# Kernel optimization log

Hardware: AMD Instinct MI355X
Metric: run time of the kernel (lower is better)

Reference implementation:

```python
import jax, jax.numpy as jnp
import numpy as np

B, T = 1, 2048
N_EMBD = 2048
N_HEAD = 16
HEAD_DIM = 128
Q_COMP = 1536
KV_COMP = 512
ROT = 64  # rotate_dim


def setup_inputs() -> dict:
    key = jax.random.key(0)
    ks = jax.random.split(key, 12)
    nrm = lambda k, shp, sc=1.0: jax.random.normal(k, shp, jnp.float32) * sc
    return {
        "x": nrm(ks[0], (B, T, N_EMBD)),
        "cos": jax.random.uniform(ks[1], (T, ROT // 2), jnp.float32),
        "sin": jax.random.uniform(ks[2], (T, ROT // 2), jnp.float32),
        "Wq_d_w": nrm(ks[3], (Q_COMP, N_EMBD), 0.02),
        "Wq_d_b": jnp.zeros((Q_COMP,), jnp.float32),
        "Wkv_d_w": nrm(ks[4], (KV_COMP, N_EMBD), 0.02),
        "Wq_u_w": nrm(ks[5], (N_HEAD * HEAD_DIM, Q_COMP), 0.02),
        "Wk_u_w": nrm(ks[6], (N_HEAD * HEAD_DIM, KV_COMP), 0.02),
        "Wv_u_w": nrm(ks[7], (N_HEAD * HEAD_DIM, KV_COMP), 0.02),
        "W_qr_w": nrm(ks[8], (N_HEAD * ROT, Q_COMP), 0.02),
        "W_kr_w": nrm(ks[9], (ROT, N_EMBD), 0.02),
        "W_out_w": nrm(ks[10], (N_EMBD, N_HEAD * HEAD_DIM), 0.02),
    }


def _rope(x, cos, sin):
    # x: [B, H, T, r]; cos/sin: [T, r//2] broadcast over batch and heads
    d = x.shape[-1] // 2
    x1, x2 = x[..., :d], x[..., d:]
    return jnp.concatenate([x1 * cos + x2 * sin, -x1 * sin + x2 * cos], axis=-1)


def reference(x, cos, sin, Wq_d_w, Wq_d_b, Wkv_d_w, Wq_u_w, Wk_u_w, Wv_u_w, W_qr_w, W_kr_w, W_out_w):
    Bn, Tn, _ = x.shape
    cq = x @ Wq_d_w.T + Wq_d_b           # [B,T,Qc] latent query
    ckv = x @ Wkv_d_w.T                  # [B,T,Kc] compressed KV latent (= K_t = V)
    Wq_u = Wq_u_w.reshape(N_HEAD, HEAD_DIM, Q_COMP)
    Wk_u = Wk_u_w.reshape(N_HEAD, HEAD_DIM, KV_COMP)
    Wv_u = Wv_u_w.reshape(N_HEAD, HEAD_DIM, KV_COMP)
    # absorbed per-head W_qk[h] = Wq_u_h^T @ Wk_u_h : [H, Qc, Kc]
    W_qk = jnp.einsum('hdq,hdk->hqk', Wq_u, Wk_u)
    Q_t = jnp.einsum('btq,hqk->bhtk', cq, W_qk)   # [B,H,T,Kc] content query in latent space
    Q_r = _rope(jnp.einsum('btq,hrq->bhtr', cq, W_qr_w.reshape(N_HEAD, ROT, Q_COMP)), cos, sin)
    K_r = _rope((x @ W_kr_w.T)[:, None], cos, sin)  # [B,1,T,R] single shared rotary key head
    Q = jnp.concatenate([Q_t, Q_r], axis=-1)        # [B,H,T,Kc+R]
    K = jnp.concatenate([ckv[:, None], K_r], axis=-1)  # [B,1,T,Kc+R]
    scale = 1.0 / np.sqrt(KV_COMP + ROT).astype(np.float32)
    scores = jnp.einsum('bhqd,bokd->bhqk', Q, K) * scale  # [B,H,T,T]
    causal = jnp.tril(jnp.ones((Tn, Tn), dtype=bool))
    scores = jnp.where(causal, scores, jnp.asarray(-1e30, scores.dtype))
    probs = jax.nn.softmax(scores, axis=-1)
    attn = jnp.einsum('bhqk,bkc->bhqc', probs, ckv)  # [B,H,T,Kc] latent attention output
    # absorbed output projection: up-project per head via Wv_u, then W_out
    heads = jnp.einsum('bhtc,hdc->bthd', attn, Wv_u).reshape(Bn, Tn, N_HEAD * HEAD_DIM)
    return heads @ W_out_w.T                          # [B,T,C]
```

## Files before the change

kernel.cpp:

```cpp
#include <hip/hip_runtime.h>
#include <math.h>
#include <stdint.h>
#include <stddef.h>

typedef __bf16 bf16;
typedef __bf16 bf16x8 __attribute__((ext_vector_type(8)));
typedef __bf16 bf16x4 __attribute__((ext_vector_type(4)));
typedef __bf16 bf16x2 __attribute__((ext_vector_type(2)));
typedef float  f32x4  __attribute__((ext_vector_type(4)));
typedef float  f32x4v __attribute__((ext_vector_type(4)));

typedef __attribute__((address_space(1))) const void* as1cv;
typedef __attribute__((address_space(3))) void*       as3v;

__device__ __forceinline__ f32x4 mfma16(bf16x8 a, bf16x8 b, f32x4 c) {
  return __builtin_amdgcn_mfma_f32_16x16x32_bf16(a, b, c, 0, 0, 0);
}

__device__ __forceinline__ void gload_lds16(const bf16* g, bf16* l) {
  __builtin_amdgcn_global_load_lds((as1cv)g, (as3v)l, 16, 0, 0);
}

struct CvtTable {
  const float* s[9];
  bf16* d[9];
  int cum[10];
};

__global__ void cvt_all(CvtTable T, int total4) {
  int i = blockIdx.x * blockDim.x + threadIdx.x;
  int stride = gridDim.x * blockDim.x;
  for (; i < total4; i += stride) {
    int k = 0;
#pragma unroll
    for (int j = 1; j < 9; ++j) k += (i >= T.cum[j]) ? 1 : 0;
    int off = i - T.cum[k];
    f32x4v v = ((const f32x4v*)T.s[k])[off];
    bf16x4 o;
    o[0] = (bf16)v[0]; o[1] = (bf16)v[1]; o[2] = (bf16)v[2]; o[3] = (bf16)v[3];
    ((bf16x4*)T.d[k])[off] = o;
  }
}

__device__ __forceinline__ void gemm_core(
    const bf16* __restrict__ A, int lda,
    const bf16* __restrict__ B, int K,
    float* __restrict__ Cf, bf16* __restrict__ Cb, int ldc,
    const float* __restrict__ bias, int bias_n, int m0, int n0)
{
  __shared__ __align__(16) bf16 Al[2][128 * 64];
  __shared__ __align__(16) bf16 Bl[2][128 * 64];
  const int tid = threadIdx.x;
  const int l = tid & 63;
  const int wid = tid >> 6;
  const int wr = wid >> 1, wc = wid & 1;
  const int lr = l & 15, lg = l >> 4;

  auto STAGE = [&](int b, int k0) {
#pragma unroll
    for (int it = 0; it < 4; ++it) {
      int chunk = it * 256 + tid;
      int row = chunk >> 3;
      int scb = (chunk & 7) ^ (row & 7);
      gload_lds16(A + (size_t)(m0 + row) * lda + k0 + scb * 8, &Al[b][chunk * 8]);
    }
#pragma unroll
    for (int it = 0; it < 4; ++it) {
      int chunk = it * 256 + tid;
      int row = chunk >> 3;
      int scb = (chunk & 7) ^ (row & 7);
      gload_lds16(B + (size_t)(n0 + row) * K + k0 + scb * 8, &Bl[b][chunk * 8]);
    }
  };

  f32x4 z = {0.f, 0.f, 0.f, 0.f};
  f32x4 acc[4][4];
#pragma unroll
  for (int i = 0; i < 4; ++i)
#pragma unroll
    for (int j = 0; j < 4; ++j) acc[i][j] = z;

  STAGE(0, 0);
  __syncthreads();
  int cur = 0;
  for (int k0 = 0; k0 < K; k0 += 64) {
    if (k0 + 64 < K) STAGE(cur ^ 1, k0 + 64);
#pragma unroll
    for (int kk = 0; kk < 2; ++kk) {
      bf16x8 af[4], bfr[4];
#pragma unroll
      for (int i = 0; i < 4; ++i) {
        int row = wr * 64 + i * 16 + lr;
        int cq = kk * 4 + lg;
        af[i] = *(const bf16x8*)(&Al[cur][row * 64 + ((cq ^ (row & 7)) * 8)]);
      }
#pragma unroll
      for (int j = 0; j < 4; ++j) {
        int row = wc * 64 + j * 16 + lr;
        int cq = kk * 4 + lg;
        bfr[j] = *(const bf16x8*)(&Bl[cur][row * 64 + ((cq ^ (row & 7)) * 8)]);
      }
#pragma unroll
      for (int i = 0; i < 4; ++i)
#pragma unroll
        for (int j = 0; j < 4; ++j)
          acc[i][j] = mfma16(af[i], bfr[j], acc[i][j]);
    }
    __syncthreads();
    cur ^= 1;
  }

#pragma unroll
  for (int i = 0; i < 4; ++i)
#pragma unroll
    for (int j = 0; j < 4; ++j)
#pragma unroll
      for (int r = 0; r < 4; ++r) {
        int row = m0 + wr * 64 + i * 16 + lg * 4 + r;
        int col = n0 + wc * 64 + j * 16 + lr;
        float v = acc[i][j][r];
        if (bias != nullptr && col < bias_n) v += bias[col];
        if (Cf != nullptr) Cf[(size_t)row * ldc + col] = v;
        else               Cb[(size_t)row * ldc + col] = (bf16)v;
      }
}

template<bool OUTF32>
__global__ __launch_bounds__(256) void gemm_bt(
    const bf16* __restrict__ A, int lda,
    const bf16* __restrict__ B, int K,
    float* __restrict__ Cf, bf16* __restrict__ Cb, int ldc,
    const float* __restrict__ bias, int bias_n)
{
  gemm_core(A, lda, B, K, OUTF32 ? Cf : nullptr, Cb, ldc, bias, bias_n,
            blockIdx.y * 128, blockIdx.x * 128);
}

__global__ __launch_bounds__(256) void gemm_bt_dual(
    const bf16* __restrict__ A0, int lda0, const bf16* __restrict__ B0, int K0,
    bf16* __restrict__ C0, int ldc0, int nbx0,
    const bf16* __restrict__ A1, int lda1, const bf16* __restrict__ B1, int K1,
    bf16* __restrict__ C1, int ldc1, int nbx1)
{
  int bid = blockIdx.x;
  if (bid < nbx0 * 16) {
    gemm_core(A0, lda0, B0, K0, nullptr, C0, ldc0, nullptr, 0,
              (bid / nbx0) * 128, (bid % nbx0) * 128);
  } else {
    bid -= nbx0 * 16;
    gemm_core(A1, lda1, B1, K1, nullptr, C1, ldc1, nullptr, 0,
              (bid / nbx1) * 128, (bid % nbx1) * 128);
  }
}

__global__ void rope_tv(const bf16* __restrict__ QA, const bf16* __restrict__ c_all,
                        const float* __restrict__ cosb, const float* __restrict__ sinb,
                        bf16* __restrict__ Qr, bf16* __restrict__ Kr,
                        const bf16* __restrict__ KV, bf16* __restrict__ Vt)
{
  int bid = blockIdx.x;
  if (bid < 2048) {
    int t = bid;
    for (int idx = threadIdx.x; idx < 544; idx += 256) {
      if (idx < 512) {
        int h = idx >> 5, p = idx & 31;
        float x1 = (float)QA[(size_t)t * 3072 + 2048 + h * 64 + p];
        float x2 = (float)QA[(size_t)t * 3072 + 2048 + h * 64 + 32 + p];
        float c = cosb[t * 32 + p], s = sinb[t * 32 + p];
        Qr[(size_t)t * 1024 + h * 64 + p]      = (bf16)( x1 * c + x2 * s);
        Qr[(size_t)t * 1024 + h * 64 + 32 + p] = (bf16)(-x1 * s + x2 * c);
      } else {
        int p = idx - 512;
        float x1 = (float)c_all[(size_t)t * 2176 + 2048 + p];
        float x2 = (float)c_all[(size_t)t * 2176 + 2048 + 32 + p];
        float c = cosb[t * 32 + p], s = sinb[t * 32 + p];
        Kr[(size_t)t * 64 + p]      = (bf16)( x1 * c + x2 * s);
        Kr[(size_t)t * 64 + 32 + p] = (bf16)(-x1 * s + x2 * c);
      }
    }
  } else {
    __shared__ bf16 tile[32][33];
    int tb = bid - 2048;
    int t0 = (tb & 63) * 32, c0 = (tb >> 6) * 32;
    int tx = threadIdx.x & 31, ty = threadIdx.x >> 5;
#pragma unroll
    for (int r = 0; r < 4; ++r)
      tile[ty + r * 8][tx] = KV[(size_t)(t0 + ty + r * 8) * 4096 + 2048 + c0 + tx];
    __syncthreads();
#pragma unroll
    for (int r = 0; r < 4; ++r)
      Vt[(size_t)(c0 + ty + r * 8) * 2048 + t0 + tx] = tile[tx][ty + r * 8];
  }
}

__global__ __launch_bounds__(256) void attn_kernel(
    const bf16* __restrict__ QA,
    const bf16* __restrict__ Qr,
    const bf16* __restrict__ KV,
    const bf16* __restrict__ Kr,
    const bf16* __restrict__ Vt,
    bf16* __restrict__ heads)
{
  __shared__ __align__(16) bf16 Kl[2][32 * 128];
  __shared__ __align__(16) bf16 Krl[2][32 * 64];
  __shared__ __align__(16) bf16 Vl[2][128 * 32];
  __shared__ __align__(16) bf16 Pl[4][16][40];

  const int tid = threadIdx.x;
  const int l = tid & 63;
  const int wid = tid >> 6;
  const int lr = l & 15, lg = l >> 4;

  const int wg = blockIdx.x;
  const int xcd = wg & 7, inx = wg >> 3;
  const int half = inx >> 5, j = inx & 31;
  const int h = xcd * 2 + half;
  const int qb = half ? j : 31 - j;
  const int q0 = qb * 64 + wid * 16;
  const int q = q0 + lr;

  const float scale = 0.041666666666666664f;
  f32x4 z = {0.f, 0.f, 0.f, 0.f};

  auto STAGE = [&](int b, int s0) {
#pragma unroll
    for (int it = 0; it < 2; ++it) {
      int ch = it * 256 + tid;
      int r = ch >> 4, p = ch & 15;
      int cb = (p & 8) | ((p & 7) ^ (r & 7));
      gload_lds16(&KV[(size_t)(s0 + r) * 4096 + h * 128 + cb * 8], &Kl[b][ch * 8]);
    }
    {
      int ch = tid;
      int r = ch >> 3, p = ch & 7;
      int cb = p ^ (r & 7);
      gload_lds16(&Kr[(size_t)(s0 + r) * 64 + cb * 8], &Krl[b][ch * 8]);
    }
#pragma unroll
    for (int it = 0; it < 2; ++it) {
      int ch = it * 256 + tid;
      int r = ch >> 2, p = ch & 3;
      int cb = p ^ ((r >> 1) & 3);
      gload_lds16(&Vt[(size_t)(h * 128 + r) * 2048 + s0 + cb * 8], &Vl[b][ch * 8]);
    }
  };

  bf16x8 aq[6];
#pragma unroll
  for (int kc = 0; kc < 4; ++kc)
    aq[kc] = *(const bf16x8*)&QA[(size_t)q * 3072 + h * 128 + kc * 32 + lg * 8];
#pragma unroll
  for (int kc = 4; kc < 6; ++kc)
    aq[kc] = *(const bf16x8*)&Qr[(size_t)q * 1024 + h * 64 + (kc - 4) * 32 + lg * 8];

  float m_run = -1e30f, l_run = 0.f;
  f32x4 acc[8];
#pragma unroll
  for (int c = 0; c < 8; ++c) acc[c] = z;

  const int nIter = 2 * qb + 2;
  STAGE(0, 0);
  __syncthreads();
  int cur = 0;
  for (int st = 0; st < nIter; ++st) {
    const int s0 = st * 32;
    if (st + 1 < nIter) STAGE(cur ^ 1, s0 + 32);
    if (s0 <= q0 + 15) {
      f32x4 sc[2];
      sc[0] = z; sc[1] = z;
#pragma unroll
      for (int t = 0; t < 2; ++t) {
        const int rr = t * 16 + lr;
#pragma unroll
        for (int kc = 0; kc < 4; ++kc) {
          int g = kc * 4 + lg;
          bf16x8 ka = *(const bf16x8*)&Kl[cur][rr * 128 + (((g & 8) | ((g & 7) ^ (rr & 7))) * 8)];
          sc[t] = mfma16(ka, aq[kc], sc[t]);
        }
#pragma unroll
        for (int kc = 4; kc < 6; ++kc) {
          int g = (kc - 4) * 4 + lg;
          bf16x8 ka = *(const bf16x8*)&Krl[cur][rr * 64 + ((g ^ (rr & 7)) * 8)];
          sc[t] = mfma16(ka, aq[kc], sc[t]);
        }
      }
      float pv[2][4];
      float mx = -1e30f;
#pragma unroll
      for (int t = 0; t < 2; ++t)
#pragma unroll
        for (int r = 0; r < 4; ++r) {
          int k = s0 + t * 16 + lg * 4 + r;
          float v = sc[t][r] * scale;
          if (k > q) v = -1e30f;
          pv[t][r] = v;
          mx = fmaxf(mx, v);
        }
      mx = fmaxf(mx, __shfl_xor(mx, 16, 64));
      mx = fmaxf(mx, __shfl_xor(mx, 32, 64));
      float mnew = fmaxf(m_run, mx);
      float alpha = __expf(m_run - mnew);
      float sum = 0.f;
#pragma unroll
      for (int t = 0; t < 2; ++t)
#pragma unroll
        for (int r = 0; r < 4; ++r) {
          float e = __expf(pv[t][r] - mnew);
          pv[t][r] = e;
          sum += e;
        }
      sum += __shfl_xor(sum, 16, 64);
      sum += __shfl_xor(sum, 32, 64);
      l_run = l_run * alpha + sum;
      m_run = mnew;
#pragma unroll
      for (int c = 0; c < 8; ++c)
#pragma unroll
        for (int r = 0; r < 4; ++r) acc[c][r] *= alpha;
#pragma unroll
      for (int t = 0; t < 2; ++t)
#pragma unroll
        for (int hf = 0; hf < 2; ++hf) {
          bf16x2 w;
          w[0] = (bf16)pv[t][2 * hf];
          w[1] = (bf16)pv[t][2 * hf + 1];
          *(bf16x2*)&Pl[wid][lr][t * 16 + lg * 4 + 2 * hf] = w;
        }
      bf16x8 pa = *(const bf16x8*)&Pl[wid][lr][lg * 8];
#pragma unroll
      for (int c = 0; c < 8; ++c) {
        int rv = c * 16 + lr;
        bf16x8 va = *(const bf16x8*)&Vl[cur][rv * 32 + ((lg ^ ((rv >> 1) & 3)) * 8)];
        acc[c] = mfma16(va, pa, acc[c]);
      }
    }
    __syncthreads();
    cur ^= 1;
  }

  const float inv = 1.f / l_run;
#pragma unroll
  for (int c = 0; c < 8; ++c) {
    bf16x4 o;
#pragma unroll
    for (int r = 0; r < 4; ++r) o[r] = (bf16)(acc[c][r] * inv);
    *(bf16x4*)&heads[(size_t)q * 2048 + h * 128 + c * 16 + lg * 4] = o;
  }
}

extern "C" void kernel_launch(void* const* d_in, const int* in_sizes, int n_in,
                              void* d_out, int out_size, void* d_ws, size_t ws_size,
                              hipStream_t stream) {
  (void)in_sizes; (void)n_in; (void)out_size; (void)ws_size;
  const float* x      = (const float*)d_in[0];
  const float* cosp   = (const float*)d_in[1];
  const float* sinp   = (const float*)d_in[2];
  const float* Wq_d   = (const float*)d_in[3];
  const float* Wq_d_b = (const float*)d_in[4];
  const float* Wkv_d  = (const float*)d_in[5];
  const float* Wq_u   = (const float*)d_in[6];
  const float* Wk_u   = (const float*)d_in[7];
  const float* Wv_u   = (const float*)d_in[8];
  const float* W_qr   = (const float*)d_in[9];
  const float* W_kr   = (const float*)d_in[10];
  const float* W_out  = (const float*)d_in[11];

  char* ws = (char*)d_ws;
  size_t off = 0;
  auto alloc = [&](size_t bytes) {
    char* p = ws + off;
    off += (bytes + 255) & ~(size_t)255;
    return p;
  };
  bf16* xb    = (bf16*)alloc((size_t)2048 * 2048 * 2);
  bf16* Wcat  = (bf16*)alloc((size_t)2176 * 2048 * 2);
  bf16* c_all = (bf16*)alloc((size_t)2048 * 2176 * 2);
  bf16* Wqu   = (bf16*)alloc((size_t)3072 * 1536 * 2);
  bf16* QA    = (bf16*)alloc((size_t)2048 * 3072 * 2);
  bf16* Wkvu  = (bf16*)alloc((size_t)4096 * 512 * 2);
  bf16* KV    = (bf16*)alloc((size_t)2048 * 4096 * 2);
  bf16* Qr    = (bf16*)alloc((size_t)2048 * 1024 * 2);
  bf16* Kr    = (bf16*)alloc((size_t)2048 * 64 * 2);
  bf16* Wout  = (bf16*)alloc((size_t)2048 * 2048 * 2);
  bf16* Vt    = xb;
  bf16* heads = Wqu;

  CvtTable T;
  const float* srcs[9] = { x, Wq_d, Wkv_d, W_kr, Wq_u, W_qr, Wk_u, Wv_u, W_out };
  bf16* dsts[9] = { xb, Wcat, Wcat + (size_t)1536 * 2048, Wcat + (size_t)2048 * 2048,
                    Wqu, Wqu + (size_t)2048 * 1536, Wkvu, Wkvu + (size_t)2048 * 512, Wout };
  size_t ns[9] = { (size_t)2048 * 2048, (size_t)1536 * 2048, (size_t)512 * 2048,
                   (size_t)64 * 2048, (size_t)2048 * 1536, (size_t)1024 * 1536,
                   (size_t)2048 * 512, (size_t)2048 * 512, (size_t)2048 * 2048 };
  int cum = 0;
  for (int i = 0; i < 9; ++i) {
    T.s[i] = srcs[i]; T.d[i] = dsts[i]; T.cum[i] = cum;
    cum += (int)(ns[i] / 4);
  }
  T.cum[9] = cum;
  cvt_all<<<2048, 256, 0, stream>>>(T, cum);

  gemm_bt<false><<<dim3(17, 16), 256, 0, stream>>>(xb, 2048, Wcat, 2048,
                                                   nullptr, c_all, 2176, Wq_d_b, 1536);
  gemm_bt_dual<<<24 * 16 + 32 * 16, 256, 0, stream>>>(
      c_all, 2176, Wqu, 1536, QA, 3072, 24,
      c_all + 1536, 2176, Wkvu, 512, KV, 4096, 32);
  rope_tv<<<2048 + 4096, 256, 0, stream>>>(QA, c_all, cosp, sinp, Qr, Kr, KV, Vt);
  attn_kernel<<<512, 256, 0, stream>>>(QA, Qr, KV, Kr, Vt, heads);
  gemm_bt<true><<<dim3(16, 16), 256, 0, stream>>>(heads, 2048, Wout, 2048,
                                                  (float*)d_out, nullptr, 2048, nullptr, 0);
}
```

Before: 340.6 us.

## Use 512-thread GEMM blocks, hoist load addresses, add lazy softmax rescaling

GEMM blocks go from 4 to 8 waves, each owning a 64x32 sub-tile, so per-wave accumulators drop from 16 to 8 MFMA tiles. Global-to-LDS staging in both the GEMM and the attention kernels now uses precomputed pointers that are advanced each step instead of recomputing addresses. In attention, the causal mask is only applied on diagonal tiles. The online-softmax rescale of the accumulators is skipped unless the running max grows by more than a threshold, which trades a little numerical headroom (exponents up to e^8 before rescaling) for fewer multiplies.

```diff
diff --git a/kernel.cpp b/kernel.cpp
--- a/kernel.cpp
+++ b/kernel.cpp
@@ -53,41 +53,44 @@
   const int tid = threadIdx.x;
   const int l = tid & 63;
   const int wid = tid >> 6;
-  const int wr = wid >> 1, wc = wid & 1;
+  const int wr = wid >> 2, wc = wid & 3;
   const int lr = l & 15, lg = l >> 4;
 
-  auto STAGE = [&](int b, int k0) {
-#pragma unroll
-    for (int it = 0; it < 4; ++it) {
-      int chunk = it * 256 + tid;
-      int row = chunk >> 3;
-      int scb = (chunk & 7) ^ (row & 7);
-      gload_lds16(A + (size_t)(m0 + row) * lda + k0 + scb * 8, &Al[b][chunk * 8]);
-    }
-#pragma unroll
-    for (int it = 0; it < 4; ++it) {
-      int chunk = it * 256 + tid;
-      int row = chunk >> 3;
-      int scb = (chunk & 7) ^ (row & 7);
-      gload_lds16(B + (size_t)(n0 + row) * K + k0 + scb * 8, &Bl[b][chunk * 8]);
-    }
+  const int ch0 = tid, ch1 = tid + 512;
+  const int ar0 = ch0 >> 3, ap0 = (ch0 & 7) ^ (ar0 & 7);
+  const int ar1 = ch1 >> 3, ap1 = (ch1 & 7) ^ (ar1 & 7);
+  const bf16* pA0 = A + (size_t)(m0 + ar0) * lda + ap0 * 8;
+  const bf16* pA1 = A + (size_t)(m0 + ar1) * lda + ap1 * 8;
+  const bf16* pB0 = B + (size_t)(n0 + ar0) * K + ap0 * 8;
+  const bf16* pB1 = B + (size_t)(n0 + ar1) * K + ap1 * 8;
+  bf16* dA0[2] = { &Al[0][ch0 * 8], &Al[1][ch0 * 8] };
+  bf16* dA1[2] = { &Al[0][ch1 * 8], &Al[1][ch1 * 8] };
+  bf16* dB0[2] = { &Bl[0][ch0 * 8], &Bl[1][ch0 * 8] };
+  bf16* dB1[2] = { &Bl[0][ch1 * 8], &Bl[1][ch1 * 8] };
+
+  auto STAGE = [&](int b) {
+    gload_lds16(pA0, b ? dA0[1] : dA0[0]);
+    gload_lds16(pA1, b ? dA1[1] : dA1[0]);
+    gload_lds16(pB0, b ? dB0[1] : dB0[0]);
+    gload_lds16(pB1, b ? dB1[1] : dB1[0]);
+    pA0 += 64; pA1 += 64; pB0 += 64; pB1 += 64;
   };
 
   f32x4 z = {0.f, 0.f, 0.f, 0.f};
-  f32x4 acc[4][4];
+  f32x4 acc[4][2];
 #pragma unroll
   for (int i = 0; i < 4; ++i)
 #pragma unroll
-    for (int j = 0; j < 4; ++j) acc[i][j] = z;
-
-  STAGE(0, 0);
+    for (int j = 0; j < 2; ++j) acc[i][j] = z;
+
+  STAGE(0);
   __syncthreads();
   int cur = 0;
   for (int k0 = 0; k0 < K; k0 += 64) {
-    if (k0 + 64 < K) STAGE(cur ^ 1, k0 + 64);
+    if (k0 + 64 < K) STAGE(cur ^ 1);
 #pragma unroll
     for (int kk = 0; kk < 2; ++kk) {
-      bf16x8 af[4], bfr[4];
+      bf16x8 af[4], bfr[2];
 #pragma unroll
       for (int i = 0; i < 4; ++i) {
         int row = wr * 64 + i * 16 + lr;
@@ -95,15 +98,15 @@
         af[i] = *(const bf16x8*)(&Al[cur][row * 64 + ((cq ^ (row & 7)) * 8)]);
       }
 #pragma unroll
-      for (int j = 0; j < 4; ++j) {
-        int row = wc * 64 + j * 16 + lr;
+      for (int j = 0; j < 2; ++j) {
+        int row = wc * 32 + j * 16 + lr;
         int cq = kk * 4 + lg;
         bfr[j] = *(const bf16x8*)(&Bl[cur][row * 64 + ((cq ^ (row & 7)) * 8)]);
       }
 #pragma unroll
       for (int i = 0; i < 4; ++i)
 #pragma unroll
-        for (int j = 0; j < 4; ++j)
+        for (int j = 0; j < 2; ++j)
           acc[i][j] = mfma16(af[i], bfr[j], acc[i][j]);
     }
     __syncthreads();
@@ -113,11 +116,11 @@
 #pragma unroll
   for (int i = 0; i < 4; ++i)
 #pragma unroll
-    for (int j = 0; j < 4; ++j)
+    for (int j = 0; j < 2; ++j)
 #pragma unroll
       for (int r = 0; r < 4; ++r) {
         int row = m0 + wr * 64 + i * 16 + lg * 4 + r;
-        int col = n0 + wc * 64 + j * 16 + lr;
+        int col = n0 + wc * 32 + j * 16 + lr;
         float v = acc[i][j][r];
         if (bias != nullptr && col < bias_n) v += bias[col];
         if (Cf != nullptr) Cf[(size_t)row * ldc + col] = v;
@@ -126,7 +129,7 @@
 }
 
 template<bool OUTF32>
-__global__ __launch_bounds__(256) void gemm_bt(
+__global__ __launch_bounds__(512) void gemm_bt(
     const bf16* __restrict__ A, int lda,
     const bf16* __restrict__ B, int K,
     float* __restrict__ Cf, bf16* __restrict__ Cb, int ldc,
@@ -136,7 +139,7 @@
             blockIdx.y * 128, blockIdx.x * 128);
 }
 
-__global__ __launch_bounds__(256) void gemm_bt_dual(
+__global__ __launch_bounds__(512) void gemm_bt_dual(
     const bf16* __restrict__ A0, int lda0, const bf16* __restrict__ B0, int K0,
     bf16* __restrict__ C0, int ldc0, int nbx0,
     const bf16* __restrict__ A1, int lda1, const bf16* __restrict__ B1, int K1,
@@ -222,27 +225,33 @@
   const float scale = 0.041666666666666664f;
   f32x4 z = {0.f, 0.f, 0.f, 0.f};
 
-  auto STAGE = [&](int b, int s0) {
-#pragma unroll
-    for (int it = 0; it < 2; ++it) {
-      int ch = it * 256 + tid;
-      int r = ch >> 4, p = ch & 15;
-      int cb = (p & 8) | ((p & 7) ^ (r & 7));
-      gload_lds16(&KV[(size_t)(s0 + r) * 4096 + h * 128 + cb * 8], &Kl[b][ch * 8]);
-    }
-    {
-      int ch = tid;
-      int r = ch >> 3, p = ch & 7;
-      int cb = p ^ (r & 7);
-      gload_lds16(&Kr[(size_t)(s0 + r) * 64 + cb * 8], &Krl[b][ch * 8]);
-    }
-#pragma unroll
-    for (int it = 0; it < 2; ++it) {
-      int ch = it * 256 + tid;
-      int r = ch >> 2, p = ch & 3;
-      int cb = p ^ ((r >> 1) & 3);
-      gload_lds16(&Vt[(size_t)(h * 128 + r) * 2048 + s0 + cb * 8], &Vl[b][ch * 8]);
-    }
+  const int chK0 = tid, chK1 = tid + 256;
+  const int rK0 = chK0 >> 4, pK0 = chK0 & 15;
+  const int rK1 = chK1 >> 4, pK1 = chK1 & 15;
+  const int cbK0 = (pK0 & 8) | ((pK0 & 7) ^ (rK0 & 7));
+  const int cbK1 = (pK1 & 8) | ((pK1 & 7) ^ (rK1 & 7));
+  const bf16* gK0 = &KV[(size_t)rK0 * 4096 + h * 128 + cbK0 * 8];
+  const bf16* gK1 = &KV[(size_t)rK1 * 4096 + h * 128 + cbK1 * 8];
+  const int rKr = tid >> 3, pKr = tid & 7, cbKr = pKr ^ (rKr & 7);
+  const bf16* gKr = &Kr[(size_t)rKr * 64 + cbKr * 8];
+  const int chV0 = tid, chV1 = tid + 256;
+  const int rV0 = chV0 >> 2, pV0 = chV0 & 3, cbV0 = pV0 ^ ((rV0 >> 1) & 3);
+  const int rV1 = chV1 >> 2, pV1 = chV1 & 3, cbV1 = pV1 ^ ((rV1 >> 1) & 3);
+  const bf16* gV0 = &Vt[(size_t)(h * 128 + rV0) * 2048 + cbV0 * 8];
+  const bf16* gV1 = &Vt[(size_t)(h * 128 + rV1) * 2048 + cbV1 * 8];
+  bf16* dK0[2] = { &Kl[0][chK0 * 8], &Kl[1][chK0 * 8] };
+  bf16* dK1[2] = { &Kl[0][chK1 * 8], &Kl[1][chK1 * 8] };
+  bf16* dKr[2] = { &Krl[0][tid * 8], &Krl[1][tid * 8] };
+  bf16* dV0[2] = { &Vl[0][chV0 * 8], &Vl[1][chV0 * 8] };
+  bf16* dV1[2] = { &Vl[0][chV1 * 8], &Vl[1][chV1 * 8] };
+
+  auto STAGE = [&](int b) {
+    gload_lds16(gK0, b ? dK0[1] : dK0[0]);
+    gload_lds16(gK1, b ? dK1[1] : dK1[0]);
+    gload_lds16(gKr, b ? dKr[1] : dKr[0]);
+    gload_lds16(gV0, b ? dV0[1] : dV0[0]);
+    gload_lds16(gV1, b ? dV1[1] : dV1[0]);
+    gK0 += 32 * 4096; gK1 += 32 * 4096; gKr += 32 * 64; gV0 += 32; gV1 += 32;
   };
 
   bf16x8 aq[6];
@@ -259,12 +268,12 @@
   for (int c = 0; c < 8; ++c) acc[c] = z;
 
   const int nIter = 2 * qb + 2;
-  STAGE(0, 0);
+  STAGE(0);
   __syncthreads();
   int cur = 0;
   for (int st = 0; st < nIter; ++st) {
     const int s0 = st * 32;
-    if (st + 1 < nIter) STAGE(cur ^ 1, s0 + 32);
+    if (st + 1 < nIter) STAGE(cur ^ 1);
     if (s0 <= q0 + 15) {
       f32x4 sc[2];
       sc[0] = z; sc[1] = z;
@@ -286,37 +295,51 @@
       }
       float pv[2][4];
       float mx = -1e30f;
-#pragma unroll
-      for (int t = 0; t < 2; ++t)
-#pragma unroll
-        for (int r = 0; r < 4; ++r) {
-          int k = s0 + t * 16 + lg * 4 + r;
-          float v = sc[t][r] * scale;
-          if (k > q) v = -1e30f;
-          pv[t][r] = v;
-          mx = fmaxf(mx, v);
-        }
+      if (s0 + 31 > q0) {
+#pragma unroll
+        for (int t = 0; t < 2; ++t)
+#pragma unroll
+          for (int r = 0; r < 4; ++r) {
+            int k = s0 + t * 16 + lg * 4 + r;
+            float v = sc[t][r] * scale;
+            if (k > q) v = -1e30f;
+            pv[t][r] = v;
+            mx = fmaxf(mx, v);
+          }
+      } else {
+#pragma unroll
+        for (int t = 0; t < 2; ++t)
+#pragma unroll
+          for (int r = 0; r < 4; ++r) {
+            float v = sc[t][r] * scale;
+            pv[t][r] = v;
+            mx = fmaxf(mx, v);
+          }
+      }
       mx = fmaxf(mx, __shfl_xor(mx, 16, 64));
       mx = fmaxf(mx, __shfl_xor(mx, 32, 64));
-      float mnew = fmaxf(m_run, mx);
-      float alpha = __expf(m_run - mnew);
+      if (!__all(mx - m_run <= 8.f)) {
+        float mnew = fmaxf(m_run, mx);
+        float alpha = __expf(m_run - mnew);
+        l_run *= alpha;
+#pragma unroll
+        for (int c = 0; c < 8; ++c)
+#pragma unroll
+          for (int r = 0; r < 4; ++r) acc[c][r] *= alpha;
+        m_run = mnew;
+      }
       float sum = 0.f;
 #pragma unroll
       for (int t = 0; t < 2; ++t)
 #pragma unroll
         for (int r = 0; r < 4; ++r) {
-          float e = __expf(pv[t][r] - mnew);
+          float e = __expf(pv[t][r] - m_run);
           pv[t][r] = e;
           sum += e;
         }
       sum += __shfl_xor(sum, 16, 64);
       sum += __shfl_xor(sum, 32, 64);
-      l_run = l_run * alpha + sum;
-      m_run = mnew;
-#pragma unroll
-      for (int c = 0; c < 8; ++c)
-#pragma unroll
-        for (int r = 0; r < 4; ++r) acc[c][r] *= alpha;
+      l_run += sum;
 #pragma unroll
       for (int t = 0; t < 2; ++t)
 #pragma unroll
@@ -400,13 +423,13 @@
   T.cum[9] = cum;
   cvt_all<<<2048, 256, 0, stream>>>(T, cum);
 
-  gemm_bt<false><<<dim3(17, 16), 256, 0, stream>>>(xb, 2048, Wcat, 2048,
+  gemm_bt<false><<<dim3(17, 16), 512, 0, stream>>>(xb, 2048, Wcat, 2048,
                                                    nullptr, c_all, 2176, Wq_d_b, 1536);
-  gemm_bt_dual<<<24 * 16 + 32 * 16, 256, 0, stream>>>(
+  gemm_bt_dual<<<24 * 16 + 32 * 16, 512, 0, stream>>>(
       c_all, 2176, Wqu, 1536, QA, 3072, 24,
       c_all + 1536, 2176, Wkvu, 512, KV, 4096, 32);
   rope_tv<<<2048 + 4096, 256, 0, stream>>>(QA, c_all, cosp, sinp, Qr, Kr, KV, Vt);
   attn_kernel<<<512, 256, 0, stream>>>(QA, Qr, KV, Kr, Vt, heads);
-  gemm_bt<true><<<dim3(16, 16), 256, 0, stream>>>(heads, 2048, Wout, 2048,
+  gemm_bt<true><<<dim3(16, 16), 512, 0, stream>>>(heads, 2048, Wout, 2048,
                                                   (float*)d_out, nullptr, 2048, nullptr, 0);
 }
```

Result: faster. 305.8 us (-10.2%).
